# Performance work log

Hardware: AMD Instinct MI355X
Metric: run time of the kernel (lower is better)

Reference implementation:

```python
import jax, jax.numpy as jnp
import numpy as np

EPS = 1e-5
NC = 183  # num_classes
FUSION_LEVEL = 1

def conv2d(x, w, b=None, pad=0):
    y = jax.lax.conv_general_dilated(x, w, (1, 1), [(pad, pad), (pad, pad)],
                                     dimension_numbers=('NCHW', 'OIHW', 'NCHW'))
    return y if b is None else y + b[None, :, None, None]

def bn(x, g, b, m, v):
    s = g / jnp.sqrt(v + EPS)
    return x * s[None, :, None, None] + (b - m * s)[None, :, None, None]

def deform_conv(x, offset, weight):
    # DCNv1: x [B,C,H,W], offset [B,18,H,W] as (dy,dx) per kernel point, weight [O,C,3,3]
    B, C, H, W = x.shape
    K = 9
    off = offset.reshape(B, K, 2, H, W)
    ky = (jnp.arange(K) // 3 - 1).astype(x.dtype)
    kx = (jnp.arange(K) % 3 - 1).astype(x.dtype)
    yy = jnp.arange(H, dtype=x.dtype)[None, None, :, None] + ky[None, :, None, None] + off[:, :, 0]
    xx = jnp.arange(W, dtype=x.dtype)[None, None, None, :] + kx[None, :, None, None] + off[:, :, 1]
    y0 = jnp.floor(yy)
    x0 = jnp.floor(xx)
    wy = yy - y0
    wx = xx - x0
    def gather(yi, xi):
        valid = ((yi >= 0) & (yi <= H - 1) & (xi >= 0) & (xi <= W - 1))
        yc = jnp.clip(yi, 0, H - 1).astype(jnp.int32)
        xc = jnp.clip(xi, 0, W - 1).astype(jnp.int32)
        g = jax.vmap(lambda im, a, b: im[:, a, b])(x, yc, xc)  # [B,C,K,H,W]
        return g * valid.astype(x.dtype)[:, None]
    s = (gather(y0, x0) * ((1 - wy) * (1 - wx))[:, None]
         + gather(y0, x0 + 1) * ((1 - wy) * wx)[:, None]
         + gather(y0 + 1, x0) * (wy * (1 - wx))[:, None]
         + gather(y0 + 1, x0 + 1) * (wy * wx)[:, None])
    return jnp.einsum('bckhw,ock->bohw', s, weight.reshape(weight.shape[0], C, K))

def resize_bilinear(x, oh, ow):
    # F.interpolate(mode='bilinear', align_corners=True)
    B, C, H, W = x.shape
    if (H, W) == (oh, ow):
        return x
    ys = jnp.linspace(0.0, H - 1.0, oh)
    xs = jnp.linspace(0.0, W - 1.0, ow)
    y0 = jnp.clip(jnp.floor(ys).astype(jnp.int32), 0, H - 2)
    x0 = jnp.clip(jnp.floor(xs).astype(jnp.int32), 0, W - 2)
    wy = (ys - y0).astype(x.dtype)
    wx = (xs - x0).astype(x.dtype)
    r = x[:, :, y0, :] * (1 - wy)[None, None, :, None] + x[:, :, y0 + 1, :] * wy[None, None, :, None]
    return r[:, :, :, x0] * (1 - wx) + r[:, :, :, x0 + 1] * wx

def setup_inputs() -> dict:
    key = jax.random.key(0)
    ks = iter(jax.random.split(key, 64))
    nk = lambda: next(ks)
    B, C = 1, 256
    sizes = [256, 128, 64, 32, 16]
    w = lambda shape, sc: jax.random.normal(nk(), shape, jnp.float32) * sc
    inp = {}
    for i, s in enumerate(sizes):
        inp['feat%d' % i] = jax.random.normal(nk(), (B, C, s, s), jnp.float32)
    inp['off1_w'] = w((18, C, 3, 3), 0.01); inp['off1_b'] = w((18,), 0.01)
    inp['dc1_w'] = w((C, C, 3, 3), 0.02)
    inp['off2_w'] = w((18, C, 3, 3), 0.01); inp['off2_b'] = w((18,), 0.01)
    inp['dc2_w'] = w((C, C, 3, 3), 0.02)
    inp['bn2_g'] = 1.0 + w((C,), 0.01); inp['bn2_b'] = w((C,), 0.01)
    inp['bn2_m'] = w((C,), 0.01); inp['bn2_v'] = jax.random.uniform(nk(), (C,), jnp.float32) + 0.5
    inp['convs_w'] = w((4, C, C, 3, 3), 0.02)
    inp['convs_g'] = 1.0 + w((4, C), 0.01); inp['convs_b'] = w((4, C), 0.01)
    inp['convs_m'] = w((4, C), 0.01); inp['convs_v'] = jax.random.uniform(nk(), (4, C), jnp.float32) + 0.5
    inp['emb_w'] = w((C, C, 1, 1), 0.05)
    inp['emb_g'] = 1.0 + w((C,), 0.01); inp['emb_b'] = w((C,), 0.01)
    inp['emb_m'] = w((C,), 0.01); inp['emb_v'] = jax.random.uniform(nk(), (C,), jnp.float32) + 0.5
    inp['logit_w'] = w((NC, C, 1, 1), 0.05); inp['logit_b'] = w((NC,), 0.01)
    return inp

def reference(feat0, feat1, feat2, feat3, feat4,
              off1_w, off1_b, dc1_w, off2_w, off2_b, dc2_w,
              bn2_g, bn2_b, bn2_m, bn2_v,
              convs_w, convs_g, convs_b, convs_m, convs_v,
              emb_w, emb_g, emb_b, emb_m, emb_v,
              logit_w, logit_b):
    feats = [feat0, feat1, feat2, feat3, feat4]
    def branch(f):
        o = conv2d(f, off1_w, off1_b, pad=1)
        h = deform_conv(f, o, dc1_w)
        o = conv2d(h, off2_w, off2_b, pad=1)
        h = deform_conv(h, o, dc2_w)
        return jax.nn.relu(bn(h, bn2_g, bn2_b, bn2_m, bn2_v))
    x = branch(feats[FUSION_LEVEL])
    H, W = x.shape[-2:]
    for i, f in enumerate(feats):
        if i != FUSION_LEVEL:
            x = x + branch(resize_bilinear(f, H, W))
    for i in range(4):
        x = jax.nn.relu(bn(conv2d(x, convs_w[i], pad=1),
                           convs_g[i], convs_b[i], convs_m[i], convs_v[i]))
    mask_pred = conv2d(x, logit_w, logit_b, pad=0)
    emb = jax.nn.relu(bn(conv2d(x, emb_w, pad=0), emb_g, emb_b, emb_m, emb_v))
    return (mask_pred, emb)
```

## Files before the change

kernel.cpp:

```cpp
#include <hip/hip_runtime.h>
#include <hip/hip_bf16.h>
#include <stdint.h>

#define EPS_BN 1e-5f
constexpr int PP = 16384;
using short8 = __attribute__((ext_vector_type(8))) short;
using f32x4  = __attribute__((ext_vector_type(4))) float;
typedef unsigned short u16;

__device__ inline float bf2f(u16 u) {
  unsigned v = ((unsigned)u) << 16; float f; __builtin_memcpy(&f, &v, 4); return f;
}
__device__ inline u16 f2bf(float f) {
  unsigned b; __builtin_memcpy(&b, &f, 4);
  b += 0x7FFFu + ((b >> 16) & 1u);
  return (u16)(b >> 16);
}
__device__ inline float u2f(unsigned x) { float f; __builtin_memcpy(&f, &x, 4); return f; }

#define GLD16(g, l) __builtin_amdgcn_global_load_lds( \
    (__attribute__((address_space(1))) void*)(void*)(g), \
    (__attribute__((address_space(3))) void*)(void*)(l), 16, 0, 0)

__global__ void bn_prep_k(const float* __restrict__ g0, const float* __restrict__ b0,
                          const float* __restrict__ m0, const float* __restrict__ v0,
                          const float* __restrict__ cg, const float* __restrict__ cb,
                          const float* __restrict__ cm, const float* __restrict__ cv,
                          const float* __restrict__ eg, const float* __restrict__ eb,
                          const float* __restrict__ em, const float* __restrict__ ev,
                          float* __restrict__ scale, float* __restrict__ shift) {
  int c = threadIdx.x;
  float s = g0[c] * rsqrtf(v0[c] + EPS_BN);
  scale[c] = s; shift[c] = b0[c] - m0[c] * s;
#pragma unroll
  for (int i = 0; i < 4; ++i) {
    float si = cg[i*256+c] * rsqrtf(cv[i*256+c] + EPS_BN);
    scale[(1+i)*256+c] = si; shift[(1+i)*256+c] = cb[i*256+c] - cm[i*256+c]*si;
  }
  float se = eg[c] * rsqrtf(ev[c] + EPS_BN);
  scale[5*256+c] = se; shift[5*256+c] = eb[c] - em[c]*se;
}

__global__ void prep_w_k(const float* __restrict__ w, u16* __restrict__ W2,
                         int Ocnt, int KK, int NPAD) {
  int idx = blockIdx.x * 256 + threadIdx.x;
  int total = NPAD * KK * 256;
  if (idx >= total) return;
  int o = idx / (KK * 256); int rem = idx - o * (KK * 256);
  int kpt = rem >> 8, c = rem & 255;
  W2[idx] = (o < Ocnt) ? f2bf(w[(o * 256 + c) * KK + kpt]) : (u16)0;
}

__global__ void prep_wf_k(const float* __restrict__ w, u16* __restrict__ W2f) {
  int idx = blockIdx.x * 256 + threadIdx.x;
  int ks = idx >> 13, r = idx & 8191;
  int n = r >> 9, r2 = r & 511;
  int lane = r2 >> 3, j = r2 & 7;
  int k = ks * 32 + ((lane >> 4) << 3) + j;
  int oc = n * 16 + (lane & 15);
  W2f[idx] = f2bf(w[(oc * 256 + (k & 255)) * 9 + (k >> 8)]);
}

__global__ void tr_k(const float* __restrict__ in, u16* __restrict__ out, int P) {
  __shared__ float tile[64][65];
  int p0 = blockIdx.x * 64, c0 = blockIdx.y * 64;
  int t = threadIdx.x;
  int tl = t & 63, tg = t >> 6;
#pragma unroll
  for (int i = 0; i < 16; ++i) {
    int c = tg * 16 + i;
    tile[c][tl] = in[(size_t)(c0 + c) * P + p0 + tl];
  }
  __syncthreads();
  int px = t >> 2, cq = t & 3;
#pragma unroll
  for (int pass = 0; pass < 2; ++pass) {
    int c = cq * 8 + pass * 32;
    u16 r[8];
#pragma unroll
    for (int j = 0; j < 8; ++j) r[j] = f2bf(tile[c + j][px]);
    *(short8*)(out + (size_t)(p0 + px) * 256 + c0 + c) = *(short8*)r;
  }
}

__global__ void rs_k(const u16* __restrict__ in, u16* __restrict__ out, int Hs) {
  int t = threadIdx.x;
  int p = blockIdx.x * 8 + (t >> 5), q = t & 31;
  int oy = p >> 7, ox = p & 127;
  float sc = (float)(Hs - 1) / 127.0f;
  float ys = oy * sc, xs = ox * sc;
  int y0 = (int)ys; if (y0 > Hs - 2) y0 = Hs - 2;
  int x0 = (int)xs; if (x0 > Hs - 2) x0 = Hs - 2;
  float wy = ys - (float)y0, wx = xs - (float)x0;
  const u16* b00 = in + ((size_t)(y0 * Hs + x0)) * 256 + q * 8;
  short8 v00 = *(const short8*)b00;
  short8 v01 = *(const short8*)(b00 + 256);
  short8 v10 = *(const short8*)(b00 + (size_t)Hs * 256);
  short8 v11 = *(const short8*)(b00 + (size_t)Hs * 256 + 256);
  u16 r[8];
#pragma unroll
  for (int j = 0; j < 8; ++j) {
    float a = bf2f((u16)v00[j]) * (1.f - wx) + bf2f((u16)v01[j]) * wx;
    float b = bf2f((u16)v10[j]) * (1.f - wx) + bf2f((u16)v11[j]) * wx;
    r[j] = f2bf(a * (1.f - wy) + b * wy);
  }
  *(short8*)(out + (size_t)p * 256 + q * 8) = *(short8*)r;
}

template<int EPI>
__launch_bounds__(256, 4)
__global__ void dc_k(const u16* __restrict__ A, const u16* __restrict__ Bw2,
                     const float* __restrict__ offs, u16* __restrict__ oB,
                     const float* __restrict__ scale, const float* __restrict__ shift) {
  __shared__ u16 sB[3][256 * 32];
  const int t = threadIdx.x, w = t >> 6, l = t & 63, lr = l & 15, lq = l >> 4;
  int bx = blockIdx.x; { int n8 = gridDim.x >> 3; bx = (bx & 7) * n8 + (bx >> 3); }
  const int p0 = bx * 64;
  const int gp = p0 + w * 16 + lr;
  const int pl = gp & 16383;
  const unsigned lbo = (unsigned)(gp & ~16383) * 256u;

  f32x4 acc[16];
#pragma unroll
  for (int n = 0; n < 16; ++n) acc[n] = (f32x4){0.f, 0.f, 0.f, 0.f};

  float wgt[4];
  unsigned cbo[4];
  short8 cv[4];

  auto newKpt = [&](int kpt) {
    float2 o2 = *(const float2*)(offs + (size_t)gp * 32 + 2 * kpt);
    float yy = (float)((pl >> 7) + kpt / 3 - 1) + o2.x;
    float xx = (float)((pl & 127) + kpt % 3 - 1) + o2.y;
    float yf = floorf(yy), xf = floorf(xx);
    float fy = yy - yf, fx = xx - xf;
    int y0 = (int)yf, x0 = (int)xf;
    float gy0 = (1.f - fy) * (((unsigned)y0 < 128u) ? 1.f : 0.f);
    float gy1 = fy * (((unsigned)(y0 + 1) < 128u) ? 1.f : 0.f);
    float gx0 = (1.f - fx) * (((unsigned)x0 < 128u) ? 1.f : 0.f);
    float gx1 = fx * (((unsigned)(x0 + 1) < 128u) ? 1.f : 0.f);
    int y0c = y0 < 0 ? 0 : (y0 > 127 ? 127 : y0);
    int y1c = y0 + 1 < 0 ? 0 : (y0 + 1 > 127 ? 127 : y0 + 1);
    int x0c = x0 < 0 ? 0 : (x0 > 127 ? 127 : x0);
    int x1c = x0 + 1 < 0 ? 0 : (x0 + 1 > 127 ? 127 : x0 + 1);
    wgt[0] = gy0 * gx0; wgt[1] = gy0 * gx1; wgt[2] = gy1 * gx0; wgt[3] = gy1 * gx1;
    cbo[0] = lbo + (unsigned)((y0c << 7) + x0c) * 256u;
    cbo[1] = lbo + (unsigned)((y0c << 7) + x1c) * 256u;
    cbo[2] = lbo + (unsigned)((y1c << 7) + x0c) * 256u;
    cbo[3] = lbo + (unsigned)((y1c << 7) + x1c) * 256u;
  };
  auto loadC = [&](int ks) {
    int cc = ((ks & 7) << 5) + lq * 8;
#pragma unroll
    for (int c = 0; c < 4; ++c)
      cv[c] = *(const short8*)(A + (size_t)cbo[c] + cc);
  };
  auto stageB = [&](int ks) {
    const u16* src = Bw2 + (size_t)ks * 8192 + t * 8;
    char* dst = (char*)sB[ks % 3] + t * 16;
#pragma unroll
    for (int it = 0; it < 4; ++it) GLD16(src + it * 2048, dst + it * 4096);
  };

  stageB(0);
  newKpt(0);
  loadC(0);

  for (int ks = 0; ks < 72; ++ks) {
    if (ks < 71) stageB(ks + 1);
    short8 af;
    {
      u16 rr[8];
      const unsigned* u0 = (const unsigned*)&cv[0];
      const unsigned* u1 = (const unsigned*)&cv[1];
      const unsigned* u2 = (const unsigned*)&cv[2];
      const unsigned* u3 = (const unsigned*)&cv[3];
#pragma unroll
      for (int j2 = 0; j2 < 4; ++j2) {
        unsigned a0 = u0[j2], a1 = u1[j2], a2 = u2[j2], a3 = u3[j2];
        float lo = wgt[0] * u2f(a0 << 16) + wgt[1] * u2f(a1 << 16)
                 + wgt[2] * u2f(a2 << 16) + wgt[3] * u2f(a3 << 16);
        float hi = wgt[0] * u2f(a0 & 0xFFFF0000u) + wgt[1] * u2f(a1 & 0xFFFF0000u)
                 + wgt[2] * u2f(a2 & 0xFFFF0000u) + wgt[3] * u2f(a3 & 0xFFFF0000u);
        __hip_bfloat16 hl = __float2bfloat16(lo);
        __hip_bfloat16 hh = __float2bfloat16(hi);
        rr[2 * j2]     = *(u16*)&hl;
        rr[2 * j2 + 1] = *(u16*)&hh;
      }
      af = *(short8*)rr;
    }
    if (ks < 71 && (((ks + 1) & 7) == 0)) newKpt((ks + 1) >> 3);
    __builtin_amdgcn_sched_barrier(0);
    __builtin_amdgcn_s_barrier();
    __builtin_amdgcn_sched_barrier(0);
    if (ks < 71) loadC(ks + 1);
    const char* base = (const char*)sB[ks % 3] + l * 16;
    __builtin_amdgcn_s_setprio(1);
#pragma unroll
    for (int n = 0; n < 16; ++n) {
      short8 bfr = *(const short8*)(base + n * 1024);
      acc[n] = __builtin_amdgcn_mfma_f32_16x16x32_bf16(af, bfr, acc[n], 0, 0, 0);
    }
    __builtin_amdgcn_s_setprio(0);
  }

  {
    int prow = p0 + w * 16 + lq * 4;
#pragma unroll
    for (int n = 0; n < 16; ++n) {
      int oc = n * 16 + lr;
      float sc = 1.f, sh = 0.f;
      if constexpr (EPI == 3) { sc = scale[oc]; sh = shift[oc]; }
#pragma unroll
      for (int q = 0; q < 4; ++q) {
        float v = acc[n][q];
        if constexpr (EPI == 3) v = fmaxf(v * sc + sh, 0.f);
        oB[(size_t)(prow + q) * 256 + oc] = f2bf(v);
      }
    }
  }
}

template<int MODE, int AM, int AN, int MW, int NW, int EPI>
__launch_bounds__(MW*NW*64)
__global__ void mm_k(const u16* __restrict__ A, const u16* __restrict__ B,
                     const u16* __restrict__ zbuf,
                     float* __restrict__ oF, u16* __restrict__ oB,
                     const float* __restrict__ bias,
                     const float* __restrict__ scale, const float* __restrict__ shift,
                     int Ktot, int ksteps, int OutN) {
  constexpr int BM = MW * AM * 16, BN = NW * AN * 16, NT = MW * NW * 64;
  constexpr int AITS = BM * 8 / NT, BITS = BN * 8 / NT;
  __shared__ u16 sA[BM * 64];
  __shared__ u16 sB[BN * 64];
  char* sAb = (char*)sA; char* sBb = (char*)sB;
  const int t = threadIdx.x;
  const int w = t >> 6, l = t & 63;
  const int lr = l & 15, lq = l >> 4;
  const int wm = w / NW, wn = w % NW;
  int bx = blockIdx.x;
  { int n8 = gridDim.x >> 3; bx = (bx & 7) * n8 + (bx >> 3); }
  const int p0 = bx * BM, n0 = blockIdx.y * BN;

  f32x4 acc[AM][AN];
#pragma unroll
  for (int m = 0; m < AM; ++m)
#pragma unroll
    for (int n = 0; n < AN; ++n) acc[m][n] = (f32x4){0.f, 0.f, 0.f, 0.f};

  for (int ks = 0; ks < ksteps; ++ks) {
    int k0 = ks * 64;
#pragma unroll
    for (int it = 0; it < BITS; ++it) {
      int ch = it * NT + t;
      int row = ch >> 3, cl = (ch & 7) ^ (row & 7);
      GLD16(B + (size_t)(n0 + row) * Ktot + k0 + cl * 8, sBb + it * (NT * 16) + w * 1024);
    }
    if constexpr (MODE == 0) {
#pragma unroll
      for (int it = 0; it < AITS; ++it) {
        int ch = it * NT + t;
        int row = ch >> 3, cl = (ch & 7) ^ (row & 7);
        GLD16(A + (size_t)(p0 + row) * Ktot + k0 + cl * 8, sAb + it * (NT * 16) + w * 1024);
      }
    } else {
      int kpt = k0 >> 8, c0 = k0 & 255;
      int dy = kpt / 3 - 1, dx = kpt % 3 - 1;
#pragma unroll
      for (int it = 0; it < AITS; ++it) {
        int ch = it * NT + t;
        int row = ch >> 3, cl = (ch & 7) ^ (row & 7);
        int gp = p0 + row; int lvl = gp >> 14, pl = gp & 16383;
        int yy = (pl >> 7) + dy, xx = (pl & 127) + dx;
        const u16* src = ((unsigned)yy < 128u && (unsigned)xx < 128u)
            ? A + ((size_t)(lvl << 14) + (yy << 7) + xx) * 256 + c0 + cl * 8
            : zbuf;
        GLD16(src, sAb + it * (NT * 16) + w * 1024);
      }
    }
    __syncthreads();
    short8 af[AM], bfr[AN];
#pragma unroll
    for (int h = 0; h < 2; ++h) {
#pragma unroll
      for (int m = 0; m < AM; ++m) {
        int ar = wm * AM * 16 + m * 16 + lr;
        af[m] = *(const short8*)(sAb + ar * 128 + (((h * 4 + lq) ^ (ar & 7)) << 4));
      }
#pragma unroll
      for (int n = 0; n < AN; ++n) {
        int br = wn * AN * 16 + n * 16 + lr;
        bfr[n] = *(const short8*)(sBb + br * 128 + (((h * 4 + lq) ^ (br & 7)) << 4));
      }
#pragma unroll
      for (int m = 0; m < AM; ++m)
#pragma unroll
        for (int n = 0; n < AN; ++n)
          acc[m][n] = __builtin_amdgcn_mfma_f32_16x16x32_bf16(af[m], bfr[n], acc[m][n], 0, 0, 0);
    }
    __syncthreads();
  }

#pragma unroll
  for (int m = 0; m < AM; ++m) {
    int prow = p0 + wm * AM * 16 + m * 16 + lq * 4;
#pragma unroll
    for (int n = 0; n < AN; ++n) {
      int oc = n0 + wn * AN * 16 + n * 16 + lr;
      if constexpr (EPI == 1) {
        float bs = (oc < 18) ? bias[oc] : 0.f;
#pragma unroll
        for (int r = 0; r < 4; ++r) oF[(size_t)(prow + r) * 32 + oc] = acc[m][n][r] + bs;
      } else if constexpr (EPI == 2) {
#pragma unroll
        for (int r = 0; r < 4; ++r) oB[(size_t)(prow + r) * 256 + oc] = f2bf(acc[m][n][r]);
      } else if constexpr (EPI == 3) {
        float sc = scale[oc], sh = shift[oc];
#pragma unroll
        for (int r = 0; r < 4; ++r)
          oB[(size_t)(prow + r) * 256 + oc] = f2bf(fmaxf(acc[m][n][r] * sc + sh, 0.f));
      } else if constexpr (EPI == 4) {
        if (oc < OutN) {
          float bs = bias[oc];
          float4 v = {acc[m][n][0] + bs, acc[m][n][1] + bs, acc[m][n][2] + bs, acc[m][n][3] + bs};
          *(float4*)(oF + (size_t)oc * PP + prow) = v;
        }
      } else {
        float sc = scale[oc], sh = shift[oc];
        float4 v = {fmaxf(acc[m][n][0] * sc + sh, 0.f), fmaxf(acc[m][n][1] * sc + sh, 0.f),
                    fmaxf(acc[m][n][2] * sc + sh, 0.f), fmaxf(acc[m][n][3] * sc + sh, 0.f)};
        *(float4*)(oF + (size_t)oc * PP + prow) = v;
      }
    }
  }
}

__global__ void sum5_k(const u16* __restrict__ H2, u16* __restrict__ out) {
  size_t base = ((size_t)blockIdx.x * 256 + threadIdx.x) * 8;
  float a[8] = {0,0,0,0,0,0,0,0};
#pragma unroll
  for (int lvl = 0; lvl < 5; ++lvl) {
    short8 v = *(const short8*)(H2 + (size_t)lvl * PP * 256 + base);
#pragma unroll
    for (int j = 0; j < 8; ++j) a[j] += bf2f((u16)v[j]);
  }
  u16 r[8];
#pragma unroll
  for (int j = 0; j < 8; ++j) r[j] = f2bf(a[j]);
  *(short8*)(out + base) = *(short8*)r;
}

extern "C" void kernel_launch(void* const* d_in, const int* in_sizes, int n_in,
                              void* d_out, int out_size, void* d_ws, size_t ws_size,
                              hipStream_t stream) {
  const float* feats[5];
  for (int i = 0; i < 5; ++i) feats[i] = (const float*)d_in[i];
  int fsz[5] = {256, 128, 64, 32, 16};
  const float* off1_w = (const float*)d_in[5];
  const float* off1_b = (const float*)d_in[6];
  const float* dc1_w  = (const float*)d_in[7];
  const float* off2_w = (const float*)d_in[8];
  const float* off2_b = (const float*)d_in[9];
  const float* dc2_w  = (const float*)d_in[10];
  const float* bn2_g  = (const float*)d_in[11];
  const float* bn2_b  = (const float*)d_in[12];
  const float* bn2_m  = (const float*)d_in[13];
  const float* bn2_v  = (const float*)d_in[14];
  const float* convs_w = (const float*)d_in[15];
  const float* convs_g = (const float*)d_in[16];
  const float* convs_b = (const float*)d_in[17];
  const float* convs_m = (const float*)d_in[18];
  const float* convs_v = (const float*)d_in[19];
  const float* emb_w  = (const float*)d_in[20];
  const float* emb_g  = (const float*)d_in[21];
  const float* emb_b  = (const float*)d_in[22];
  const float* emb_m  = (const float*)d_in[23];
  const float* emb_v  = (const float*)d_in[24];
  const float* logit_w = (const float*)d_in[25];
  const float* logit_b = (const float*)d_in[26];

  char* ws = (char*)d_ws;
  size_t off = 0;
  auto alloc = [&](size_t bytes) { char* p = ws + off; off += (bytes + 255) & ~255ull; return p; };
  float* bnscale = (float*)alloc(6 * 256 * 4);
  float* bnshift = (float*)alloc(6 * 256 * 4);
  u16* zbuf = (u16*)alloc(256);
  u16* W2_off1 = (u16*)alloc((size_t)32 * 2304 * 2);
  u16* W2_off2 = (u16*)alloc((size_t)32 * 2304 * 2);
  u16* W2_dc1  = (u16*)alloc((size_t)256 * 2304 * 2);
  u16* W2_dc2  = (u16*)alloc((size_t)256 * 2304 * 2);
  u16* W2_c    = (u16*)alloc((size_t)4 * 256 * 2304 * 2);
  u16* W2_logit = (u16*)alloc((size_t)256 * 256 * 2);
  u16* W2_emb   = (u16*)alloc((size_t)256 * 256 * 2);
  u16* R_all  = (u16*)alloc((size_t)5 * PP * 256 * 2);
  u16* H_all  = (u16*)alloc((size_t)5 * PP * 256 * 2);
  u16* H2_all = (u16*)alloc((size_t)5 * PP * 256 * 2);
  float* O    = (float*)alloc((size_t)5 * PP * 32 * 4);
  u16* Xb     = (u16*)alloc((size_t)PP * 256 * 2);
  u16* Ftmp = H_all;
  u16* cb0 = R_all;
  u16* cb1 = R_all + (size_t)PP * 256;

  hipMemsetAsync(zbuf, 0, 256, stream);
  bn_prep_k<<<1, 256, 0, stream>>>(bn2_g, bn2_b, bn2_m, bn2_v, convs_g, convs_b, convs_m, convs_v,
                                   emb_g, emb_b, emb_m, emb_v, bnscale, bnshift);
  auto pw = [&](const float* src, u16* dst, int Ocnt, int KK, int NPAD) {
    int total = NPAD * KK * 256;
    prep_w_k<<<(total + 255) / 256, 256, 0, stream>>>(src, dst, Ocnt, KK, NPAD);
  };
  pw(off1_w, W2_off1, 18, 9, 32);
  pw(off2_w, W2_off2, 18, 9, 32);
  prep_wf_k<<<2304, 256, 0, stream>>>(dc1_w, W2_dc1);
  prep_wf_k<<<2304, 256, 0, stream>>>(dc2_w, W2_dc2);
  for (int i = 0; i < 4; ++i) pw(convs_w + (size_t)i * 2304 * 256, W2_c + (size_t)i * 2304 * 256, 256, 9, 256);
  pw(logit_w, W2_logit, 183, 1, 256);
  pw(emb_w,   W2_emb,   256, 1, 256);

  const dim3 blk(256);
  for (int lvl = 0; lvl < 5; ++lvl) {
    int P = fsz[lvl] * fsz[lvl];
    u16* dst = (lvl == 1) ? (R_all + (size_t)PP * 256) : Ftmp;
    tr_k<<<dim3(P / 64, 4), blk, 0, stream>>>(feats[lvl], dst, P);
    if (lvl != 1)
      rs_k<<<dim3(PP / 8), blk, 0, stream>>>(Ftmp, R_all + (size_t)lvl * PP * 256, fsz[lvl]);
  }

  constexpr int MG = 5 * PP;
  mm_k<1, 2, 2, 4, 1, 1><<<dim3(MG / 128, 1), blk, 0, stream>>>(
      R_all, W2_off1, zbuf, O, nullptr, off1_b, nullptr, nullptr, 2304, 36, 32);
  dc_k<2><<<dim3(MG / 64), blk, 0, stream>>>(R_all, W2_dc1, O, H_all, nullptr, nullptr);
  mm_k<1, 2, 2, 4, 1, 1><<<dim3(MG / 128, 1), blk, 0, stream>>>(
      H_all, W2_off2, zbuf, O, nullptr, off2_b, nullptr, nullptr, 2304, 36, 32);
  dc_k<3><<<dim3(MG / 64), blk, 0, stream>>>(H_all, W2_dc2, O, H2_all, bnscale, bnshift);

  sum5_k<<<dim3(2048), blk, 0, stream>>>(H2_all, Xb);

  const u16* cur = Xb;
  u16* cbuf[2] = {cb0, cb1};
  for (int i = 0; i < 4; ++i) {
    mm_k<1, 2, 2, 2, 2, 3><<<dim3(PP / 64, 4), blk, 0, stream>>>(
        cur, W2_c + (size_t)i * 2304 * 256, zbuf, nullptr, cbuf[i & 1],
        nullptr, bnscale + (1 + i) * 256, bnshift + (1 + i) * 256, 2304, 36, 256);
    cur = cbuf[i & 1];
  }

  float* outp = (float*)d_out;
  mm_k<0, 2, 4, 2, 2, 4><<<dim3(PP / 64, 2), blk, 0, stream>>>(
      cur, W2_logit, zbuf, outp, nullptr, logit_b, nullptr, nullptr, 256, 4, 183);
  mm_k<0, 2, 4, 2, 2, 5><<<dim3(PP / 64, 2), blk, 0, stream>>>(
      cur, W2_emb, zbuf, outp + (size_t)183 * PP, nullptr, nullptr,
      bnscale + 5 * 256, bnshift + 5 * 256, 256, 4, 256);
}
```

Measured before the change: 779.3 us.

## Deepen deform-conv prefetch to two stages with double-buffered sampling state

```diff
diff --git a/kernel.cpp b/kernel.cpp
--- a/kernel.cpp
+++ b/kernel.cpp
@@ -108,7 +108,7 @@
 }
 
 template<int EPI>
-__launch_bounds__(256, 4)
+__launch_bounds__(256, 2)
 __global__ void dc_k(const u16* __restrict__ A, const u16* __restrict__ Bw2,
                      const float* __restrict__ offs, u16* __restrict__ oB,
                      const float* __restrict__ scale, const float* __restrict__ shift) {
@@ -124,11 +124,12 @@
 #pragma unroll
   for (int n = 0; n < 16; ++n) acc[n] = (f32x4){0.f, 0.f, 0.f, 0.f};
 
-  float wgt[4];
-  unsigned cbo[4];
-  short8 cv[4];
+  float    wgt[2][4];
+  unsigned cbo[2][4];
+  short8   cv[2][4];
 
   auto newKpt = [&](int kpt) {
+    int sl = kpt & 1;
     float2 o2 = *(const float2*)(offs + (size_t)gp * 32 + 2 * kpt);
     float yy = (float)((pl >> 7) + kpt / 3 - 1) + o2.x;
     float xx = (float)((pl & 127) + kpt % 3 - 1) + o2.y;
@@ -143,17 +144,19 @@
     int y1c = y0 + 1 < 0 ? 0 : (y0 + 1 > 127 ? 127 : y0 + 1);
     int x0c = x0 < 0 ? 0 : (x0 > 127 ? 127 : x0);
     int x1c = x0 + 1 < 0 ? 0 : (x0 + 1 > 127 ? 127 : x0 + 1);
-    wgt[0] = gy0 * gx0; wgt[1] = gy0 * gx1; wgt[2] = gy1 * gx0; wgt[3] = gy1 * gx1;
-    cbo[0] = lbo + (unsigned)((y0c << 7) + x0c) * 256u;
-    cbo[1] = lbo + (unsigned)((y0c << 7) + x1c) * 256u;
-    cbo[2] = lbo + (unsigned)((y1c << 7) + x0c) * 256u;
-    cbo[3] = lbo + (unsigned)((y1c << 7) + x1c) * 256u;
+    wgt[sl][0] = gy0 * gx0; wgt[sl][1] = gy0 * gx1;
+    wgt[sl][2] = gy1 * gx0; wgt[sl][3] = gy1 * gx1;
+    cbo[sl][0] = lbo + (unsigned)((y0c << 7) + x0c) * 256u;
+    cbo[sl][1] = lbo + (unsigned)((y0c << 7) + x1c) * 256u;
+    cbo[sl][2] = lbo + (unsigned)((y1c << 7) + x0c) * 256u;
+    cbo[sl][3] = lbo + (unsigned)((y1c << 7) + x1c) * 256u;
   };
-  auto loadC = [&](int ks) {
-    int cc = ((ks & 7) << 5) + lq * 8;
+  auto loadC = [&](int s) {
+    int sl = (s >> 3) & 1;
+    int cc = ((s & 7) << 5) + lq * 8;
 #pragma unroll
     for (int c = 0; c < 4; ++c)
-      cv[c] = *(const short8*)(A + (size_t)cbo[c] + cc);
+      cv[s & 1][c] = *(const short8*)(A + (size_t)cbo[sl][c] + cc);
   };
   auto stageB = [&](int ks) {
     const u16* src = Bw2 + (size_t)ks * 8192 + t * 8;
@@ -162,26 +165,26 @@
     for (int it = 0; it < 4; ++it) GLD16(src + it * 2048, dst + it * 4096);
   };
 
-  stageB(0);
   newKpt(0);
-  loadC(0);
+  stageB(0); loadC(0);
+  stageB(1); loadC(1);
 
   for (int ks = 0; ks < 72; ++ks) {
-    if (ks < 71) stageB(ks + 1);
     short8 af;
     {
+      const float* wg = wgt[(ks >> 3) & 1];
       u16 rr[8];
-      const unsigned* u0 = (const unsigned*)&cv[0];
-      const unsigned* u1 = (const unsigned*)&cv[1];
-      const unsigned* u2 = (const unsigned*)&cv[2];
-      const unsigned* u3 = (const unsigned*)&cv[3];
+      const unsigned* u0 = (const unsigned*)&cv[ks & 1][0];
+      const unsigned* u1 = (const unsigned*)&cv[ks & 1][1];
+      const unsigned* u2 = (const unsigned*)&cv[ks & 1][2];
+      const unsigned* u3 = (const unsigned*)&cv[ks & 1][3];
 #pragma unroll
       for (int j2 = 0; j2 < 4; ++j2) {
         unsigned a0 = u0[j2], a1 = u1[j2], a2 = u2[j2], a3 = u3[j2];
-        float lo = wgt[0] * u2f(a0 << 16) + wgt[1] * u2f(a1 << 16)
-                 + wgt[2] * u2f(a2 << 16) + wgt[3] * u2f(a3 << 16);
-        float hi = wgt[0] * u2f(a0 & 0xFFFF0000u) + wgt[1] * u2f(a1 & 0xFFFF0000u)
-                 + wgt[2] * u2f(a2 & 0xFFFF0000u) + wgt[3] * u2f(a3 & 0xFFFF0000u);
+        float lo = wg[0] * u2f(a0 << 16) + wg[1] * u2f(a1 << 16)
+                 + wg[2] * u2f(a2 << 16) + wg[3] * u2f(a3 << 16);
+        float hi = wg[0] * u2f(a0 & 0xFFFF0000u) + wg[1] * u2f(a1 & 0xFFFF0000u)
+                 + wg[2] * u2f(a2 & 0xFFFF0000u) + wg[3] * u2f(a3 & 0xFFFF0000u);
         __hip_bfloat16 hl = __float2bfloat16(lo);
         __hip_bfloat16 hh = __float2bfloat16(hi);
         rr[2 * j2]     = *(u16*)&hl;
@@ -189,11 +192,14 @@
       }
       af = *(short8*)rr;
     }
-    if (ks < 71 && (((ks + 1) & 7) == 0)) newKpt((ks + 1) >> 3);
     __builtin_amdgcn_sched_barrier(0);
     __builtin_amdgcn_s_barrier();
     __builtin_amdgcn_sched_barrier(0);
-    if (ks < 71) loadC(ks + 1);
+    if (ks < 70) {
+      if (((ks + 2) & 7) == 0) newKpt((ks + 2) >> 3);
+      stageB(ks + 2);
+      loadC(ks + 2);
+    }
     const char* base = (const char*)sB[ks % 3] + l * 16;
     __builtin_amdgcn_s_setprio(1);
 #pragma unroll
```

Measured after the change: 1.380 ms. 1.77x slower.
